# Kernel tuning notes

Measured on AMD Instinct MI355X. Metric: run time of the kernel, lower is better.

Reference implementation:

```python
import jax, jax.numpy as jnp
import numpy as np

NODE = 400      # number of ROIs
POP = 3         # populations: ['E','I','P']  (P index = 2)
STATE = 4       # V, gE, gI, gNMDA
TRS = 40        # TRs_per_window
STEPS = 10      # steps_per_TR = int(tr/step_size) = int(1.0/0.1)
DT = 0.1        # step_size
OUT = 64        # EEG channels
DMAX = 500      # delays_max buffer length

# theta layout (relu applied in reference as in torch forward):
# 0:VL 1:VI 2:VE 3:VNMDA 4:alpha_mg 5:VR 6:pi_sigma 7:gL 8:C 9:kappa
# 10:gamma_gE 11:gamma_gE_sc 12:gamma_gI 13:gamma_gI_sc 14:gamma_gNMDA
# 15:gamma_gNMDA_sc 16:gamma_k 17:sigma_V 18:sigma_g 19:y0 20:mu_raw
# 21:k 22:cy0 23:ki 24:g 25:g_f 26:g_b

def setup_inputs() -> dict:
    key = jax.random.key(0)
    ks = jax.random.split(key, 8)
    external = 0.1 * jax.random.normal(ks[0], (NODE, STEPS, TRS), jnp.float32)
    # createIC: uniform(-1,1) + [-60, 64, 64, 64]
    hx = jax.random.uniform(ks[1], (NODE, POP, STATE), jnp.float32, -1.0, 1.0) \
         + jnp.array([-60.0, 64.0, 64.0, 64.0], jnp.float32)
    # createDelayIC: uniform(-0.2, 0.2)
    hE = jax.random.uniform(ks[2], (NODE, DMAX), jnp.float32, -0.2, 0.2)
    A = jax.random.uniform(ks[3], (NODE, NODE), jnp.float32)
    sc = 0.5 * (A + A.T)
    sc = sc.at[jnp.arange(NODE), jnp.arange(NODE)].set(0.0)
    D = 100.0 * jax.random.uniform(ks[4], (NODE, NODE), jnp.float32)
    dist = 0.5 * (D + D.T)
    dist = dist.at[jnp.arange(NODE), jnp.arange(NODE)].set(0.0)
    w0 = jnp.full((NODE, NODE), 0.05, jnp.float32)  # setModelParameters init
    lm = jax.random.normal(ks[5], (OUT, NODE), jnp.float32)
    theta = jnp.array([60.0, 80.0, 60.0, 60.0, 0.06, 0.0, 0.1, 1.0, 100.0, 0.5,
                       5.0, 5.0, 5.0, 5.0, 2.0, 2.0, 5.0, 0.1, 0.1, 2.0, 0.9,
                       1.0, 6.0, 1.0, 10.0, 1.0, 1.0], jnp.float32)
    return {"external": external, "hx": hx, "hE": hE, "sc": sc, "dist": dist,
            "w_bb": w0, "w_ff": w0, "w_ll": w0, "lm": lm, "theta": theta}


def reference(external, hx, hE, sc, dist, w_bb, w_ff, w_ll, lm, theta):
    r = jax.nn.relu
    VL, VI, VE, VNMDA = r(theta[0]), r(theta[1]), r(theta[2]), r(theta[3])
    alpha_mg, VR, pi_sigma = r(theta[4]), r(theta[5]), r(theta[6])
    gL, C, kappa = r(theta[7]), r(theta[8]), r(theta[9])
    gamma_gE, gamma_gE_sc = r(theta[10]), r(theta[11])
    gamma_gI, gamma_gI_sc = r(theta[12]), r(theta[13])
    gamma_gNMDA, gamma_gNMDA_sc = r(theta[14]), r(theta[15])
    gamma_k = r(theta[16])
    y0 = theta[19]
    mu = 0.1 + r(theta[20])
    k = r(theta[21])
    cy0, ki = theta[22], theta[23]
    g_l, g_f, g_b = r(theta[24]), r(theta[25]), r(theta[26])

    # SC-modulated, norm-scaled gain matrices (as in forward body)
    w_b = jnp.exp(w_bb) * sc
    w_n_b = w_b / jnp.linalg.norm(w_b)
    rs_b = w_n_b.sum(1)                      # diag of -dg_b
    w_f = jnp.exp(w_ff) * sc
    w_n_f = w_f / jnp.linalg.norm(w_f)
    rs_f = w_n_f.sum(1)
    w = jnp.exp(w_ll) * sc
    ws = 0.5 * (w + w.T)
    w_n_l = ws / jnp.linalg.norm(ws)
    rs_l = w_n_l.sum(1)

    delays = jnp.clip((dist / mu).astype(jnp.int32), 0, DMAX - 1)  # [N,N]
    lm_d = lm - lm.mean(axis=0, keepdims=True)  # demeaned leadfield
    dt = jnp.float32(DT)

    def step_fn(carry, u_t):
        V, gE, gI, gNMDA, hEbuf = carry
        s = jax.nn.sigmoid(pi_sigma * (V - VR))  # firing rates [N,3]
        sE, sI, sP = s[:, 0], s[:, 1], s[:, 2]
        # delayed P firing gathered per (target,source) pair
        Ed = jnp.take_along_axis(hEbuf, delays, axis=1)  # [N,N]
        lr_l = g_l * ((w_n_l * Ed).sum(1) - rs_l * sP)   # LEd + dg_l @ sP
        lr_f = g_f * ((w_n_f * Ed).sum(1) - rs_f * sP)
        lr_b = g_b * ((w_n_b * Ed).sum(1) - rs_b * sP)
        u = k * ki * u_t                                  # external drive [N]
        exc = jnp.stack([gamma_gE * sP + lr_l + u,
                         gamma_gE_sc * sE + lr_b,
                         gamma_k * sE + lr_f + u], axis=1)
        inh = jnp.stack([gamma_gI * sI, gamma_gI_sc * sI, gamma_gI * sI], axis=1)
        nmda = jnp.stack([gamma_gNMDA * sP + lr_l,
                          gamma_gNMDA_sc * sE,
                          gamma_gNMDA * sE], axis=1)
        mN = 1.0 / (1.0 + 0.2 * jnp.exp(-alpha_mg * V))   # m_nmda
        dV = (gL * (-VL - V) + gE * (VE - V) + gI * (-VI - V)
              + gNMDA * mN * (VNMDA - V)) / C
        V2 = V + dt * dV
        gE2 = gE + dt * kappa * (exc - gE)
        gI2 = gI + dt * kappa * (inh - gI)
        gN2 = gNMDA + dt * kappa * (nmda - gNMDA)
        hE2 = jnp.concatenate([s[:, 2:3], hEbuf[:, :-1]], axis=1)
        return (V2, gE2, gI2, gN2, hE2), None

    def tr_fn(carry, u_tr):  # u_tr: [STEPS, N]
        carry, _ = jax.lax.scan(step_fn, carry, u_tr)
        V = carry[0]
        eeg = cy0 * (lm_d @ V[:, 2]) - y0  # [OUT]
        return carry, eeg

    u_all = jnp.transpose(external, (2, 1, 0))  # [TRS, STEPS, N]
    carry0 = (hx[:, :, 0], hx[:, :, 1], hx[:, :, 2], hx[:, :, 3], hE)
    _, eeg = jax.lax.scan(tr_fn, carry0, u_all)
    return eeg  # [TRS, OUT]
```

## Files before the change

kernel.cpp:

```cpp
#include <hip/hip_runtime.h>
#include <type_traits>

#define NODE 400
#define POP 3
#define TRS 40
#define STEPS 10
#define DMAX 500
#define OUT 64
#define DT 0.1f
#define JPL 7
#define WSTR 512

__device__ __forceinline__ float relu_(float x) { return x > 0.f ? x : 0.f; }
__device__ __forceinline__ float rcp_(float x) { return __builtin_amdgcn_rcpf(x); }
__device__ __forceinline__ float rlane_(float v, int l) {
  return __builtin_bit_cast(float, __builtin_amdgcn_readlane(__builtin_bit_cast(int, v), l));
}
__device__ __forceinline__ float bperm0_(float v) {
  return __builtin_bit_cast(float,
      __builtin_amdgcn_ds_bpermute(0, __builtin_bit_cast(int, v)));
}
template <int OFF>
__device__ __forceinline__ float swz_(float v) {
  return __builtin_bit_cast(float,
      __builtin_amdgcn_ds_swizzle(__builtin_bit_cast(int, v), OFF));
}
#define PIN_V(x) asm volatile("" : "+v"(x))

template <int CTRL>
__device__ __forceinline__ float dpp_mov(float x) {
  int r = __builtin_amdgcn_update_dpp(0, __builtin_bit_cast(int, x), CTRL,
                                      0xf, 0xf, true);
  return __builtin_bit_cast(float, r);
}
template <int CTRL>
__device__ __forceinline__ int dpp_movi(int x) {
  return __builtin_amdgcn_update_dpp(0, x, CTRL, 0xf, 0xf, true);
}
__device__ __forceinline__ float wrol1(float x) { return dpp_mov<0x134>(x); }

__device__ __forceinline__ void wave_reduce3(float& a, float& b, float& c) {
  a += dpp_mov<0x111>(a); b += dpp_mov<0x111>(b); c += dpp_mov<0x111>(c);
  a += dpp_mov<0x112>(a); b += dpp_mov<0x112>(b); c += dpp_mov<0x112>(c);
  a += dpp_mov<0x114>(a); b += dpp_mov<0x114>(b); c += dpp_mov<0x114>(c);
  a += dpp_mov<0x118>(a); b += dpp_mov<0x118>(b); c += dpp_mov<0x118>(c);
  a += dpp_mov<0x142>(a); b += dpp_mov<0x142>(b); c += dpp_mov<0x142>(c);
  a += dpp_mov<0x143>(a); b += dpp_mov<0x143>(b); c += dpp_mov<0x143>(c);
  a = rlane_(a, 63); b = rlane_(b, 63); c = rlane_(c, 63);
}

__device__ __forceinline__ float wave_reduce1(float a) {
  a += dpp_mov<0x111>(a); a += dpp_mov<0x112>(a); a += dpp_mov<0x114>(a);
  a += dpp_mov<0x118>(a); a += dpp_mov<0x142>(a); a += dpp_mov<0x143>(a);
  return rlane_(a, 63);
}

__device__ __forceinline__ int wave_max_int(int x) {
  x = max(x, dpp_movi<0x111>(x));
  x = max(x, dpp_movi<0x112>(x));
  x = max(x, dpp_movi<0x114>(x));
  x = max(x, dpp_movi<0x118>(x));
  x = max(x, dpp_movi<0x142>(x));
  x = max(x, dpp_movi<0x143>(x));
  return __builtin_amdgcn_readlane(x, 63);
}

__global__ __launch_bounds__(256) void ssq_kernel(
    const float* __restrict__ wbb, const float* __restrict__ wff,
    const float* __restrict__ wll, const float* __restrict__ sc,
    float* __restrict__ part) {
  float eb = 0.f, ef = 0.f, el = 0.f;
  for (int idx = blockIdx.x * 256 + threadIdx.x; idx < NODE * NODE;
       idx += 64 * 256) {
    int i = idx / NODE, j = idx - i * NODE;
    int ji = j * NODE + i;
    float scij = sc[idx];
    float b = expf(wbb[idx]) * scij;
    float f = expf(wff[idx]) * scij;
    float l = 0.5f * (expf(wll[idx]) * scij + expf(wll[ji]) * sc[ji]);
    eb = fmaf(b, b, eb); ef = fmaf(f, f, ef); el = fmaf(l, l, el);
  }
  wave_reduce3(eb, ef, el);
  __shared__ float red[3][4];
  int lane = threadIdx.x & 63, wv = threadIdx.x >> 6;
  if (lane == 0) { red[0][wv] = eb; red[1][wv] = ef; red[2][wv] = el; }
  __syncthreads();
  if (threadIdx.x == 0) {
    part[blockIdx.x]       = red[0][0] + red[0][1] + red[0][2] + red[0][3];
    part[64 + blockIdx.x]  = red[1][0] + red[1][1] + red[1][2] + red[1][3];
    part[128 + blockIdx.x] = red[2][0] + red[2][1] + red[2][2] + red[2][3];
  }
}

__global__ __launch_bounds__(128) void sim_kernel(
    const float* __restrict__ external, const float* __restrict__ hx,
    const float* __restrict__ hE, const float* __restrict__ sc,
    const float* __restrict__ dist, const float* __restrict__ wbb,
    const float* __restrict__ wff, const float* __restrict__ wll,
    const float* __restrict__ theta, const float* __restrict__ part,
    float* __restrict__ vsnap) {
  const int wv = threadIdx.x >> 6;
  const int lane = threadIdx.x & 63;
  const int node = blockIdx.x * 2 + wv;

  __shared__ float Wall[2][3 * WSTR];
  __shared__ float hE_lds[2][DMAX];
  __shared__ float u_lds[2][STEPS * TRS];
  __shared__ float sc_c[2][3];
  __shared__ int   sc_md[2];

  float sb = part[lane], sf = part[64 + lane], sl = part[128 + lane];
  wave_reduce3(sb, sf, sl);
  const float inv_nb = 1.f / sqrtf(sb);
  const float inv_nf = 1.f / sqrtf(sf);
  const float inv_nl = 1.f / sqrtf(sl);

  const float VL = relu_(theta[0]), VI = relu_(theta[1]);
  const float VE = relu_(theta[2]), VNMDA = relu_(theta[3]);
  const float alpha_mg = relu_(theta[4]), VR = relu_(theta[5]);
  const float pi_sigma = relu_(theta[6]);
  const float gLp = relu_(theta[7]), Cc = relu_(theta[8]), kappa = relu_(theta[9]);
  const float g_gE = relu_(theta[10]), g_gE_sc = relu_(theta[11]);
  const float g_gI = relu_(theta[12]), g_gI_sc = relu_(theta[13]);
  const float g_gN = relu_(theta[14]), g_gN_sc = relu_(theta[15]);
  const float g_k = relu_(theta[16]);
  const float mu = 0.1f + relu_(theta[20]);
  const float uk = relu_(theta[21]) * theta[23];
  const float g_l = relu_(theta[24]), g_f = relu_(theta[25]), g_b = relu_(theta[26]);
  const float DTC = DT / Cc;
  const float dk = DT * kappa;
  const float nps = -pi_sigma, psVR = pi_sigma * VR;
  const float nam = -alpha_mg;

  const float dk1  = 1.f - dk;
  const float cA   = dk * g_l;
  const float cF   = dk * g_f;
  const float cB   = dk * g_b;
  const float cE0s = dk * g_gE;
  const float cE1e = dk * g_gE_sc;
  const float cE2e = dk * g_k;
  const float cI0  = dk * g_gI;
  const float cI1  = dk * g_gI_sc;
  const float cN0s = dk * g_gN;
  const float cN1  = dk * g_gN_sc;
  const float cN2  = dk * g_gN;
  const float gLVL = gLp * VL;
  const float L2E = 1.44269504088896f;
  const float npsL2 = nps * L2E;
  const float namL2 = nam * L2E;

  for (int k = lane; k < 3 * WSTR; k += 64) Wall[wv][k] = 0.f;
  for (int d = lane; d < DMAX; d += 64) hE_lds[wv][d] = hE[node * DMAX + d];
  const float ukdk = dk * uk;
  for (int t = lane; t < STEPS * TRS; t += 64)
    u_lds[wv][t] = ukdk * external[node * STEPS * TRS + t];

  const float scl = inv_nl * cA, scf = inv_nf * cF, scb = inv_nb * cB;
  float rl = 0.f, rf = 0.f, rb = 0.f;
  int mymax = 0;
#pragma unroll
  for (int kj = 0; kj < JPL; ++kj) {
    int j = lane + kj * 64;
    if (j < NODE) {
      int ij = node * NODE + j;
      int ji = j * NODE + node;
      float scij = sc[ij];
      float vb = expf(wbb[ij]) * scij * scb;
      float vf = expf(wff[ij]) * scij * scf;
      float vl = 0.5f * (expf(wll[ij]) * scij + expf(wll[ji]) * sc[ji]) * scl;
      int dd = (int)(dist[ij] / mu);
      dd = min(max(dd, 0), DMAX - 1);
      atomicAdd(&Wall[wv][dd], vl);
      atomicAdd(&Wall[wv][WSTR + dd], vf);
      atomicAdd(&Wall[wv][2 * WSTR + dd], vb);
      rl += vl; rf += vf; rb += vb;
      mymax = max(mymax, dd);
    }
  }
  wave_reduce3(rl, rf, rb);
  const int maxd_w = wave_max_int(mymax);
  if (lane == 0) {
    sc_c[wv][0] = rl; sc_c[wv][1] = rf; sc_c[wv][2] = rb;
    sc_md[wv] = maxd_w;
  }
  __syncthreads();
  const int maxd = max(sc_md[0], sc_md[1]);

  if (maxd <= 126) {
    if (wv != 0) return;
    const int h = lane >> 5, hlane = lane & 31;
    const int nodeF = blockIdx.x * 2 + h;
    const int p3 = hlane % 3;
    const bool isP1 = (p3 == 1), isP2 = (p3 == 2), isP0 = (p3 == 0);

    const float rlh = sc_c[h][0], rfh = sc_c[h][1], rbh = sc_c[h][2];
    const float cE0s2 = cE0s - rlh;
    const float cN0s2 = cN0s - rlh;
    const float cE1s = -rbh;
    const float cE2s = -rfh;
    const float aE = isP1 ? cE1e : (isP2 ? cE2e : 0.f);
    const float bE = isP1 ? cE1s : (isP2 ? cE2s : cE0s2);
    const float uflag = isP1 ? 0.f : 1.f;
    const float cI = isP1 ? cI1 : cI0;
    const float pN = isP0 ? cN0s2 : 0.f;
    const float qN = isP1 ? cN1 : (isP2 ? cN2 : 0.f);
    float vngLVL = -gLVL;       PIN_V(vngLVL);
    float vpsVRL2 = psVR * L2E; PIN_V(vpsVRL2);

    const bool htop = (hlane == 31);
    constexpr int NR = 4;

    float Wshl[NR], Wshf[NR], Wshb[NR];
    const float W0l = Wall[h][0], W0f = Wall[h][WSTR], W0b = Wall[h][2 * WSTR];
    const float hE0 = hE_lds[h][0];
#pragma unroll
    for (int r = 0; r < NR; ++r) {
      int s = NR * hlane + r + 1;
      Wshl[r] = Wall[h][s];
      Wshf[r] = Wall[h][WSTR + s];
      Wshb[r] = Wall[h][2 * WSTR + s];
    }

    const float inv_dk1 = 1.f / dk1;
    const int hb = nodeF * POP * 4 + 4 * p3;
    float V = hx[hb + 0];
    float E = (hx[hb + 1] - bE * hE0) * inv_dk1;
    float I = hx[hb + 2] * inv_dk1;
    float N = (hx[hb + 3] - pN * hE0) * inv_dk1;

    float Ql[NR], Qf[NR], Qb[NR], hbuf[NR];
#pragma unroll
    for (int r = 0; r < NR; ++r) { Ql[r] = 0.f; Qf[r] = 0.f; Qb[r] = 0.f; hbuf[r] = 0.f; }
    for (int d = 0; d <= maxd; ++d) {
      float wl_ = Wall[h][d], wf_ = Wall[h][WSTR + d], wb_ = Wall[h][2 * WSTR + d];
#pragma unroll
      for (int r = NR - 1; r > 0; --r) hbuf[r] = hbuf[r - 1];
      int idx = d - NR * hlane;
      bool ok = idx >= 0;
      float hv = hE_lds[h][ok ? idx : 0];
      hbuf[0] = ok ? hv : 0.f;
#pragma unroll
      for (int r = 0; r < NR; ++r) {
        Ql[r] = fmaf(wl_, hbuf[r], Ql[r]);
        Qf[r] = fmaf(wf_, hbuf[r], Qf[r]);
        Qb[r] = fmaf(wb_, hbuf[r], Qb[r]);
      }
    }
#pragma unroll
    for (int r = 0; r < NR; ++r) {
      int s = NR * hlane + r;
      Ql[r] = fmaf(-Wall[h][s], hE0, Ql[r]);
      Qf[r] = fmaf(-Wall[h][WSTR + s], hE0, Qf[r]);
      Qb[r] = fmaf(-Wall[h][2 * WSTR + s], hE0, Qb[r]);
    }

    const float* uh = &u_lds[h][0];
    float bsE = 0.f, bsI = 0.f, bsP = hE0;
    float bt2 = 0.f, bt3 = 0.f, t1c = 0.f, carryU = 0.f;

    for (int tr = 0; tr < TRS; ++tr) {
      float uu[STEPS];
#pragma unroll
      for (int s2 = 0; s2 < STEPS; ++s2) uu[s2] = uh[s2 * TRS + tr];
#pragma unroll
      for (int st = 0; st < STEPS; ++st) {
        float Uprev = (st == 0) ? carryU : uu[st - 1];
        float sg = rcp_(1.f + __builtin_amdgcn_exp2f(fmaf(npsL2, V, vpsVRL2)));
        float mm = rcp_(fmaf(0.2f, __builtin_amdgcn_exp2f(namL2 * V), 1.f));
        float t1n = fmaf(W0l, bsP, Ql[0]);
        float t2n = fmaf(W0f, bsP, Qf[0]);
        float t3n = fmaf(W0b, bsP, Qb[0]);
        float nbsE = swz_<(0 << 5)>(sg);
        float nbsI = swz_<(1 << 5)>(sg);
        float nbsP = swz_<(2 << 5)>(sg);
        float nbt2 = swz_<(0 << 5)>(t2n);
        float nbt3 = swz_<(0 << 5)>(t3n);
        __builtin_amdgcn_sched_barrier(0);
        {
          float tE = isP1 ? bt3 : (isP2 ? bt2 : t1c);
          float tN = isP0 ? t1c : 0.f;
          E = fmaf(dk1, E, fmaf(aE, bsE, fmaf(bE, bsP, fmaf(uflag, Uprev, tE))));
          I = fmaf(dk1, I, cI * bsI);
          N = fmaf(dk1, N, fmaf(pN, bsP, fmaf(qN, bsE, tN)));
        }
        float Nm = N * mm;
        float R = fmaf(E, VE, fmaf(Nm, VNMDA, fmaf(I, -VI, vngLVL)));
        float S = ((gLp + E) + I) + Nm;
        V = fmaf(DTC, fmaf(-S, V, R), V);
        float nll = wrol1(Ql[0]); nll = htop ? 0.f : nll;
        float nlf = wrol1(Qf[0]); nlf = htop ? 0.f : nlf;
        float nlb = wrol1(Qb[0]); nlb = htop ? 0.f : nlb;
        Ql[0] = fmaf(Wshl[0], bsP, Ql[1]);
        Ql[1] = fmaf(Wshl[1], bsP, Ql[2]);
        Ql[2] = fmaf(Wshl[2], bsP, Ql[3]);
        Ql[3] = fmaf(Wshl[3], bsP, nll);
        Qf[0] = fmaf(Wshf[0], bsP, Qf[1]);
        Qf[1] = fmaf(Wshf[1], bsP, Qf[2]);
        Qf[2] = fmaf(Wshf[2], bsP, Qf[3]);
        Qf[3] = fmaf(Wshf[3], bsP, nlf);
        Qb[0] = fmaf(Wshb[0], bsP, Qb[1]);
        Qb[1] = fmaf(Wshb[1], bsP, Qb[2]);
        Qb[2] = fmaf(Wshb[2], bsP, Qb[3]);
        Qb[3] = fmaf(Wshb[3], bsP, nlb);
        bsE = nbsE; bsI = nbsI; bsP = nbsP; bt2 = nbt2; bt3 = nbt3;
        t1c = t1n;
      }
      carryU = uu[STEPS - 1];
      if (hlane == 2) vsnap[tr * NODE + nodeF] = V;
    }
    return;
  }

  {
    const float cE0s2 = cE0s - rl;
    const float cN0s2 = cN0s - rl;
    const float cE1s = -rb;
    const float cE2s = -rf;

    const int hb = node * POP * 4;
    float V0 = hx[hb + 0], V1 = hx[hb + 4], V2 = hx[hb + 8];
    float E0 = hx[hb + 1], E1 = hx[hb + 5], E2 = hx[hb + 9];
    float I0 = hx[hb + 2], I1 = hx[hb + 6], I2 = hx[hb + 10];
    float N0 = hx[hb + 3], N1 = hx[hb + 7], N2 = hx[hb + 11];

    const bool loS = (lane < 3);
    const float caL = loS ? npsL2 : namL2;
    const float cbL = loS ? psVR * L2E : 0.f;
    const float cdL = loS ? 1.f : 0.2f;
    const bool selB = (lane == 1) || (lane == 4);
    const bool selC = (lane == 2) || (lane == 5);
    const bool is63 = (lane == 63);

    float vE0s2 = cE0s2; PIN_V(vE0s2);
    float vN0s2 = cN0s2; PIN_V(vN0s2);
    float vE1e  = cE1e;  PIN_V(vE1e);
    float vE1s  = cE1s;  PIN_V(vE1s);
    float vE2e  = cE2e;  PIN_V(vE2e);
    float vE2s  = cE2s;  PIN_V(vE2s);
    float vI0   = cI0;   PIN_V(vI0);
    float vI1   = cI1;   PIN_V(vI1);
    float vN1   = cN1;   PIN_V(vN1);
    float vN2   = cN2;   PIN_V(vN2);
    float vngLVL = -gLVL; PIN_V(vngLVL);

    constexpr int NR = 8;
    float Wl[NR], Wf[NR], Wb[NR];
#pragma unroll
    for (int r = 0; r < NR; ++r) {
      int s = NR * lane + r;
      Wl[r] = Wall[wv][s];
      Wf[r] = Wall[wv][WSTR + s];
      Wb[r] = Wall[wv][2 * WSTR + s];
    }

    float Pl[NR], Pf[NR], Pb[NR], hbuf[NR];
#pragma unroll
    for (int r = 0; r < NR; ++r) { Pl[r] = 0.f; Pf[r] = 0.f; Pb[r] = 0.f; hbuf[r] = 0.f; }
    for (int d = 0; d <= maxd; ++d) {
      float wl_ = Wall[wv][d], wf_ = Wall[wv][WSTR + d], wb_ = Wall[wv][2 * WSTR + d];
#pragma unroll
      for (int r = NR - 1; r > 0; --r) hbuf[r] = hbuf[r - 1];
      int idx = d - NR * lane;
      bool ok = idx >= 0;
      float hv = hE_lds[wv][ok ? idx : 0];
      hbuf[0] = ok ? hv : 0.f;
#pragma unroll
      for (int r = 0; r < NR; ++r) {
        Pl[r] = fmaf(wl_, hbuf[r], Pl[r]);
        Pf[r] = fmaf(wf_, hbuf[r], Pf[r]);
        Pb[r] = fmaf(wb_, hbuf[r], Pb[r]);
      }
    }

    auto rotscat = [&](float* P, const float* W, float sPv) {
      float nl = is63 ? 0.f : wrol1(P[0]);
#pragma unroll
      for (int r = 0; r < NR - 1; ++r) P[r] = fmaf(W[r], sPv, P[r + 1]);
      P[NR - 1] = fmaf(W[NR - 1], sPv, nl);
    };

    for (int tr = 0; tr < TRS; ++tr) {
      float u_tr = (lane < STEPS) ? u_lds[wv][lane * TRS + tr] : 0.f;
#pragma unroll
      for (int st = 0; st < STEPS; ++st) {
        float t1 = bperm0_(Pl[0]);
        float t2 = bperm0_(Pf[0]);
        float t3 = bperm0_(Pb[0]);

        float Vs = selC ? V2 : (selB ? V1 : V0);
        float ex = __builtin_amdgcn_exp2f(fmaf(caL, Vs, cbL));
        float sg = rcp_(fmaf(cdL, ex, 1.f));
        float sE = rlane_(sg, 0), sI = rlane_(sg, 1), sP = rlane_(sg, 2);
        float m0 = rlane_(sg, 3), m1 = rlane_(sg, 4), m2 = rlane_(sg, 5);
        float U = rlane_(u_tr, st);

        float T0 = t1 + U;
        float T2 = t2 + U;
        float nE0 = fmaf(dk1, E0, fmaf(vE0s2, sP, T0));
        float nN0 = fmaf(dk1, N0, fmaf(vN0s2, sP, t1));
        float nE1 = fmaf(dk1, E1, fmaf(vE1e, sE, fmaf(vE1s, sP, t3)));
        float nN1 = fmaf(dk1, N1, vN1 * sE);
        float nE2 = fmaf(dk1, E2, fmaf(vE2e, sE, fmaf(vE2s, sP, T2)));
        float nN2 = fmaf(dk1, N2, vN2 * sE);
        float pI = vI0 * sI;
        float nI0 = fmaf(dk1, I0, pI);
        float nI1 = fmaf(dk1, I1, vI1 * sI);
        float nI2 = fmaf(dk1, I2, pI);

        float Nm0 = N0 * m0, Nm1 = N1 * m1, Nm2 = N2 * m2;
        float R0 = fmaf(E0, VE, fmaf(Nm0, VNMDA, fmaf(I0, -VI, vngLVL)));
        float R1 = fmaf(E1, VE, fmaf(Nm1, VNMDA, fmaf(I1, -VI, vngLVL)));
        float R2 = fmaf(E2, VE, fmaf(Nm2, VNMDA, fmaf(I2, -VI, vngLVL)));
        float S0 = gLp + E0 + I0 + Nm0;
        float S1 = gLp + E1 + I1 + Nm1;
        float S2 = gLp + E2 + I2 + Nm2;
        V0 = fmaf(DTC, fmaf(-S0, V0, R0), V0);
        V1 = fmaf(DTC, fmaf(-S1, V1, R1), V1);
        V2 = fmaf(DTC, fmaf(-S2, V2, R2), V2);
        E0 = nE0; E1 = nE1; E2 = nE2;
        I0 = nI0; I1 = nI1; I2 = nI2;
        N0 = nN0; N1 = nN1; N2 = nN2;

        rotscat(Pl, Wl, sP);
        rotscat(Pf, Wf, sP);
        rotscat(Pb, Wb, sP);
      }
      if (lane == 0) vsnap[tr * NODE + node] = V2;
    }
  }
}

__global__ __launch_bounds__(256) void eeg_kernel(
    const float* __restrict__ lm, const float* __restrict__ vsnap,
    const float* __restrict__ theta, float* __restrict__ out) {
  int tr = blockIdx.x;
  __shared__ float vs[NODE];
  __shared__ float partl[4][OUT];
  int tid = threadIdx.x;
  for (int n = tid; n < NODE; n += 256) vs[n] = vsnap[tr * NODE + n];
  __syncthreads();
  int o = tid & 63, w = tid >> 6;
  float acc = 0.f;
  for (int n = w * 100; n < w * 100 + 100; ++n)
    acc = fmaf(lm[o * NODE + n], vs[n], acc);
  partl[w][o] = acc;
  __syncthreads();
  if (tid < OUT) {
    float cy0 = theta[22], y0 = theta[19];
    float a = partl[0][tid] + partl[1][tid] + partl[2][tid] + partl[3][tid];
    float mean = wave_reduce1(a) * (1.f / OUT);
    out[tr * OUT + tid] = cy0 * (a - mean) - y0;
  }
}

extern "C" void kernel_launch(void* const* d_in, const int* in_sizes, int n_in,
                              void* d_out, int out_size, void* d_ws, size_t ws_size,
                              hipStream_t stream) {
  const float* external = (const float*)d_in[0];
  const float* hx       = (const float*)d_in[1];
  const float* hE       = (const float*)d_in[2];
  const float* sc       = (const float*)d_in[3];
  const float* dist     = (const float*)d_in[4];
  const float* wbb      = (const float*)d_in[5];
  const float* wff      = (const float*)d_in[6];
  const float* wll      = (const float*)d_in[7];
  const float* lm       = (const float*)d_in[8];
  const float* theta    = (const float*)d_in[9];
  float* out = (float*)d_out;

  float* vsnap = (float*)d_ws;
  float* part  = vsnap + TRS * NODE;

  ssq_kernel<<<64, 256, 0, stream>>>(wbb, wff, wll, sc, part);
  sim_kernel<<<NODE / 2, 128, 0, stream>>>(external, hx, hE, sc, dist, wbb, wff,
                                           wll, theta, part, vsnap);
  eeg_kernel<<<TRS, 256, 0, stream>>>(lm, vsnap, theta, out);
}
```

Before: 145.9 us.

## Run one node per wave in fast path using readlane broadcasts

```diff
diff --git a/kernel.cpp b/kernel.cpp
--- a/kernel.cpp
+++ b/kernel.cpp
@@ -19,11 +19,6 @@
 __device__ __forceinline__ float bperm0_(float v) {
   return __builtin_bit_cast(float,
       __builtin_amdgcn_ds_bpermute(0, __builtin_bit_cast(int, v)));
-}
-template <int OFF>
-__device__ __forceinline__ float swz_(float v) {
-  return __builtin_bit_cast(float,
-      __builtin_amdgcn_ds_swizzle(__builtin_bit_cast(int, v), OFF));
 }
 #define PIN_V(x) asm volatile("" : "+v"(x))
 
@@ -106,8 +101,6 @@
   __shared__ float Wall[2][3 * WSTR];
   __shared__ float hE_lds[2][DMAX];
   __shared__ float u_lds[2][STEPS * TRS];
-  __shared__ float sc_c[2][3];
-  __shared__ int   sc_md[2];
 
   float sb = part[lane], sf = part[64 + lane], sl = part[128 + lane];
   wave_reduce3(sb, sf, sl);
@@ -178,66 +171,61 @@
     }
   }
   wave_reduce3(rl, rf, rb);
-  const int maxd_w = wave_max_int(mymax);
-  if (lane == 0) {
-    sc_c[wv][0] = rl; sc_c[wv][1] = rf; sc_c[wv][2] = rb;
-    sc_md[wv] = maxd_w;
-  }
-  __syncthreads();
-  const int maxd = max(sc_md[0], sc_md[1]);
+  const int maxd = wave_max_int(mymax);
 
   if (maxd <= 126) {
-    if (wv != 0) return;
-    const int h = lane >> 5, hlane = lane & 31;
-    const int nodeF = blockIdx.x * 2 + h;
-    const int p3 = hlane % 3;
+    const int p3 = lane % 3;
     const bool isP1 = (p3 == 1), isP2 = (p3 == 2), isP0 = (p3 == 0);
 
-    const float rlh = sc_c[h][0], rfh = sc_c[h][1], rbh = sc_c[h][2];
-    const float cE0s2 = cE0s - rlh;
-    const float cN0s2 = cN0s - rlh;
-    const float cE1s = -rbh;
-    const float cE2s = -rfh;
+    const float cE0s2 = cE0s - rl;
+    const float cN0s2 = cN0s - rl;
+    const float cE1s = -rb;
+    const float cE2s = -rf;
     const float aE = isP1 ? cE1e : (isP2 ? cE2e : 0.f);
     const float bE = isP1 ? cE1s : (isP2 ? cE2s : cE0s2);
     const float uflag = isP1 ? 0.f : 1.f;
     const float cI = isP1 ? cI1 : cI0;
     const float pN = isP0 ? cN0s2 : 0.f;
     const float qN = isP1 ? cN1 : (isP2 ? cN2 : 0.f);
+    const float fT1 = isP0 ? 1.f : 0.f;
+    const float fT2 = isP2 ? 1.f : 0.f;
+    const float fT3 = isP1 ? 1.f : 0.f;
     float vngLVL = -gLVL;       PIN_V(vngLVL);
     float vpsVRL2 = psVR * L2E; PIN_V(vpsVRL2);
-
-    const bool htop = (hlane == 31);
-    constexpr int NR = 4;
-
-    float Wshl[NR], Wshf[NR], Wshb[NR];
-    const float W0l = Wall[h][0], W0f = Wall[h][WSTR], W0b = Wall[h][2 * WSTR];
-    const float hE0 = hE_lds[h][0];
-#pragma unroll
-    for (int r = 0; r < NR; ++r) {
-      int s = NR * hlane + r + 1;
-      Wshl[r] = Wall[h][s];
-      Wshf[r] = Wall[h][WSTR + s];
-      Wshb[r] = Wall[h][2 * WSTR + s];
-    }
+    float vW0l = Wall[wv][0];        PIN_V(vW0l);
+    float vW0f = Wall[wv][WSTR];     PIN_V(vW0f);
+    float vW0b = Wall[wv][2 * WSTR]; PIN_V(vW0b);
+    const float hE0 = hE_lds[wv][0];
 
     const float inv_dk1 = 1.f / dk1;
-    const int hb = nodeF * POP * 4 + 4 * p3;
+    const int hb = node * POP * 4 + 4 * p3;
     float V = hx[hb + 0];
     float E = (hx[hb + 1] - bE * hE0) * inv_dk1;
     float I = hx[hb + 2] * inv_dk1;
     float N = (hx[hb + 3] - pN * hE0) * inv_dk1;
 
+    const bool wtop = (lane == 63);
+    constexpr int NR = 2;
+
+    float Wshl[NR], Wshf[NR], Wshb[NR];
+#pragma unroll
+    for (int r = 0; r < NR; ++r) {
+      int s = NR * lane + r + 1;
+      Wshl[r] = Wall[wv][s];
+      Wshf[r] = Wall[wv][WSTR + s];
+      Wshb[r] = Wall[wv][2 * WSTR + s];
+    }
+
     float Ql[NR], Qf[NR], Qb[NR], hbuf[NR];
 #pragma unroll
     for (int r = 0; r < NR; ++r) { Ql[r] = 0.f; Qf[r] = 0.f; Qb[r] = 0.f; hbuf[r] = 0.f; }
     for (int d = 0; d <= maxd; ++d) {
-      float wl_ = Wall[h][d], wf_ = Wall[h][WSTR + d], wb_ = Wall[h][2 * WSTR + d];
+      float wl_ = Wall[wv][d], wf_ = Wall[wv][WSTR + d], wb_ = Wall[wv][2 * WSTR + d];
 #pragma unroll
       for (int r = NR - 1; r > 0; --r) hbuf[r] = hbuf[r - 1];
-      int idx = d - NR * hlane;
+      int idx = d - NR * lane;
       bool ok = idx >= 0;
-      float hv = hE_lds[h][ok ? idx : 0];
+      float hv = hE_lds[wv][ok ? idx : 0];
       hbuf[0] = ok ? hv : 0.f;
 #pragma unroll
       for (int r = 0; r < NR; ++r) {
@@ -248,15 +236,15 @@
     }
 #pragma unroll
     for (int r = 0; r < NR; ++r) {
-      int s = NR * hlane + r;
-      Ql[r] = fmaf(-Wall[h][s], hE0, Ql[r]);
-      Qf[r] = fmaf(-Wall[h][WSTR + s], hE0, Qf[r]);
-      Qb[r] = fmaf(-Wall[h][2 * WSTR + s], hE0, Qb[r]);
-    }
-
-    const float* uh = &u_lds[h][0];
+      int s = NR * lane + r;
+      Ql[r] = fmaf(-Wall[wv][s], hE0, Ql[r]);
+      Qf[r] = fmaf(-Wall[wv][WSTR + s], hE0, Qf[r]);
+      Qb[r] = fmaf(-Wall[wv][2 * WSTR + s], hE0, Qb[r]);
+    }
+
+    const float* uh = &u_lds[wv][0];
     float bsE = 0.f, bsI = 0.f, bsP = hE0;
-    float bt2 = 0.f, bt3 = 0.f, t1c = 0.f, carryU = 0.f;
+    float st1 = 0.f, st2 = 0.f, st3 = 0.f, carryU = 0.f;
 
     for (int tr = 0; tr < TRS; ++tr) {
       float uu[STEPS];
@@ -267,46 +255,38 @@
         float Uprev = (st == 0) ? carryU : uu[st - 1];
         float sg = rcp_(1.f + __builtin_amdgcn_exp2f(fmaf(npsL2, V, vpsVRL2)));
         float mm = rcp_(fmaf(0.2f, __builtin_amdgcn_exp2f(namL2 * V), 1.f));
-        float t1n = fmaf(W0l, bsP, Ql[0]);
-        float t2n = fmaf(W0f, bsP, Qf[0]);
-        float t3n = fmaf(W0b, bsP, Qb[0]);
-        float nbsE = swz_<(0 << 5)>(sg);
-        float nbsI = swz_<(1 << 5)>(sg);
-        float nbsP = swz_<(2 << 5)>(sg);
-        float nbt2 = swz_<(0 << 5)>(t2n);
-        float nbt3 = swz_<(0 << 5)>(t3n);
-        __builtin_amdgcn_sched_barrier(0);
-        {
-          float tE = isP1 ? bt3 : (isP2 ? bt2 : t1c);
-          float tN = isP0 ? t1c : 0.f;
-          E = fmaf(dk1, E, fmaf(aE, bsE, fmaf(bE, bsP, fmaf(uflag, Uprev, tE))));
-          I = fmaf(dk1, I, cI * bsI);
-          N = fmaf(dk1, N, fmaf(pN, bsP, fmaf(qN, bsE, tN)));
-        }
+        float t1n = fmaf(vW0l, bsP, Ql[0]);
+        float t2n = fmaf(vW0f, bsP, Qf[0]);
+        float t3n = fmaf(vW0b, bsP, Qb[0]);
+        float nbsE = rlane_(sg, 0);
+        float nbsI = rlane_(sg, 1);
+        float nbsP = rlane_(sg, 2);
+        float nst1 = rlane_(t1n, 0);
+        float nst2 = rlane_(t2n, 0);
+        float nst3 = rlane_(t3n, 0);
+        float g1 = fT1 * st1;
+        float tE = fmaf(fT3, st3, fmaf(fT2, st2, g1));
+        E = fmaf(dk1, E, fmaf(aE, bsE, fmaf(bE, bsP, fmaf(uflag, Uprev, tE))));
+        I = fmaf(dk1, I, cI * bsI);
+        N = fmaf(dk1, N, fmaf(pN, bsP, fmaf(qN, bsE, g1)));
         float Nm = N * mm;
         float R = fmaf(E, VE, fmaf(Nm, VNMDA, fmaf(I, -VI, vngLVL)));
         float S = ((gLp + E) + I) + Nm;
         V = fmaf(DTC, fmaf(-S, V, R), V);
-        float nll = wrol1(Ql[0]); nll = htop ? 0.f : nll;
-        float nlf = wrol1(Qf[0]); nlf = htop ? 0.f : nlf;
-        float nlb = wrol1(Qb[0]); nlb = htop ? 0.f : nlb;
+        float nll = wrol1(Ql[0]); nll = wtop ? 0.f : nll;
+        float nlf = wrol1(Qf[0]); nlf = wtop ? 0.f : nlf;
+        float nlb = wrol1(Qb[0]); nlb = wtop ? 0.f : nlb;
         Ql[0] = fmaf(Wshl[0], bsP, Ql[1]);
-        Ql[1] = fmaf(Wshl[1], bsP, Ql[2]);
-        Ql[2] = fmaf(Wshl[2], bsP, Ql[3]);
-        Ql[3] = fmaf(Wshl[3], bsP, nll);
+        Ql[1] = fmaf(Wshl[1], bsP, nll);
         Qf[0] = fmaf(Wshf[0], bsP, Qf[1]);
-        Qf[1] = fmaf(Wshf[1], bsP, Qf[2]);
-        Qf[2] = fmaf(Wshf[2], bsP, Qf[3]);
-        Qf[3] = fmaf(Wshf[3], bsP, nlf);
+        Qf[1] = fmaf(Wshf[1], bsP, nlf);
         Qb[0] = fmaf(Wshb[0], bsP, Qb[1]);
-        Qb[1] = fmaf(Wshb[1], bsP, Qb[2]);
-        Qb[2] = fmaf(Wshb[2], bsP, Qb[3]);
-        Qb[3] = fmaf(Wshb[3], bsP, nlb);
-        bsE = nbsE; bsI = nbsI; bsP = nbsP; bt2 = nbt2; bt3 = nbt3;
-        t1c = t1n;
+        Qb[1] = fmaf(Wshb[1], bsP, nlb);
+        bsE = nbsE; bsI = nbsI; bsP = nbsP;
+        st1 = nst1; st2 = nst2; st3 = nst3;
       }
       carryU = uu[STEPS - 1];
-      if (hlane == 2) vsnap[tr * NODE + nodeF] = V;
+      if (lane == 2) vsnap[tr * NODE + node] = V;
     }
     return;
   }
```

Result: faster. 137.3 us (-5.9%).
